# Performance work log

Measured on AMD Instinct MI355X. Metric: run time of the kernel, lower is better.

The kernel has to match this reference:

```python
import jax, jax.numpy as jnp
import numpy as np

D_MODEL = 1024
NUM_HEADS = 16
HEAD_DIM = D_MODEL // NUM_HEADS


def setup_inputs() -> dict:
    key = jax.random.key(0)
    ks = jax.random.split(key, 9)
    s = 1.0 / np.sqrt(D_MODEL)
    x = jax.random.normal(ks[0], (2, 2048, D_MODEL), dtype=jnp.float32)
    Wq = jax.random.uniform(ks[1], (D_MODEL, D_MODEL), jnp.float32, -s, s)
    bq = jax.random.uniform(ks[2], (D_MODEL,), jnp.float32, -s, s)
    Wk = jax.random.uniform(ks[3], (D_MODEL, D_MODEL), jnp.float32, -s, s)
    bk = jax.random.uniform(ks[4], (D_MODEL,), jnp.float32, -s, s)
    Wv = jax.random.uniform(ks[5], (D_MODEL, D_MODEL), jnp.float32, -s, s)
    bv = jax.random.uniform(ks[6], (D_MODEL,), jnp.float32, -s, s)
    Wo = jax.random.uniform(ks[7], (D_MODEL, D_MODEL), jnp.float32, -s, s)
    bo = jax.random.uniform(ks[8], (D_MODEL,), jnp.float32, -s, s)
    return {"x": x, "Wq": Wq, "bq": bq, "Wk": Wk, "bk": bk,
            "Wv": Wv, "bv": bv, "Wo": Wo, "bo": bo}


def reference(x, Wq, bq, Wk, bk, Wv, bv, Wo, bo):
    B, S, D = x.shape
    H, Hd = NUM_HEADS, HEAD_DIM
    # projections (torch Linear: x @ W.T + b; here W stored as [in, out])
    q = (x @ Wq + bq).reshape(B, S, H, Hd).transpose(0, 2, 1, 3)  # [B,H,S,Hd]
    k = (x @ Wk + bk).reshape(B, S, H, Hd).transpose(0, 2, 1, 3)
    v = (x @ Wv + bv).reshape(B, S, H, Hd).transpose(0, 2, 1, 3)
    scale = 1.0 / jnp.sqrt(jnp.asarray(Hd, dtype=x.dtype))
    scores = jnp.einsum('bhqd,bhkd->bhqk', q, k) * scale  # [B,H,S,S]
    attn = jax.nn.softmax(scores, axis=-1)
    out = jnp.einsum('bhqk,bhkd->bhqd', attn, v)  # [B,H,S,Hd]
    out = out.transpose(0, 2, 1, 3).reshape(B, S, D)
    return out @ Wo + bo
```

## Files before the change

kernel.cpp:

```cpp
#include <hip/hip_runtime.h>
#include <hip/hip_bf16.h>
#include <string.h>


#define DM 1024
#define S_LEN 2048
#define NH 16
#define HD 64

using u16 = unsigned short;
using u32 = unsigned int;

typedef short bf16x8 __attribute__((ext_vector_type(8)));
typedef float f32x4  __attribute__((ext_vector_type(4)));
typedef float f32x16 __attribute__((ext_vector_type(16)));
typedef unsigned int u32x2 __attribute__((ext_vector_type(2)));

__device__ __forceinline__ u16 f2bf(float f) {
    u32 i = __float_as_uint(f);
    u32 r = i + 0x7fffu + ((i >> 16) & 1u);
    return (u16)(r >> 16);
}
__device__ __forceinline__ u32 pk_bf16(float a, float b) {
    __hip_bfloat162 h = __float22bfloat162_rn(float2{a, b});
    u32 r; memcpy(&r, &h, 4);
    return r;
}

__global__ __launch_bounds__(256) void prep_x(const float* __restrict__ X, u16* __restrict__ out) {
    int i = (blockIdx.x * 256 + threadIdx.x) * 4;
    float4 v = *(const float4*)(X + i);
    *(uint2*)(out + i) = make_uint2(pk_bf16(v.x, v.y), pk_bf16(v.z, v.w));
}

__global__ __launch_bounds__(256) void prep_wt3(
    const float* __restrict__ W0, const float* __restrict__ W1, const float* __restrict__ W2,
    u16* __restrict__ T0, u16* __restrict__ T1, u16* __restrict__ T2)
{
    __shared__ u16 tile[64][72];
    const float* W = (blockIdx.z == 0) ? W0 : (blockIdx.z == 1) ? W1 : W2;
    u16* WT        = (blockIdx.z == 0) ? T0 : (blockIdx.z == 1) ? T1 : T2;
    const int t = threadIdx.x;
    const int n0 = blockIdx.x * 64, k0 = blockIdx.y * 64;
    #pragma unroll
    for (int it = 0; it < 4; it++) {
        int k = it * 16 + (t >> 4);
        int n = (t & 15) * 4;
        float4 v = *(const float4*)(W + (size_t)(k0 + k) * DM + n0 + n);
        tile[n + 0][k] = f2bf(v.x);
        tile[n + 1][k] = f2bf(v.y);
        tile[n + 2][k] = f2bf(v.z);
        tile[n + 3][k] = f2bf(v.w);
    }
    __syncthreads();
    int n = t >> 2, kg = (t & 3) * 16;
    uint4 a = *(const uint4*)&tile[n][kg];
    uint4 b = *(const uint4*)&tile[n][kg + 8];
    *(uint4*)(WT + (size_t)(n0 + n) * DM + k0 + kg)     = a;
    *(uint4*)(WT + (size_t)(n0 + n) * DM + k0 + kg + 8) = b;
}

__global__ __launch_bounds__(256) void prep_wt1(const float* __restrict__ W, u16* __restrict__ WT) {
    __shared__ u16 tile[64][72];
    const int t = threadIdx.x;
    const int n0 = blockIdx.x * 64, k0 = blockIdx.y * 64;
    #pragma unroll
    for (int it = 0; it < 4; it++) {
        int k = it * 16 + (t >> 4);
        int n = (t & 15) * 4;
        float4 v = *(const float4*)(W + (size_t)(k0 + k) * DM + n0 + n);
        tile[n + 0][k] = f2bf(v.x);
        tile[n + 1][k] = f2bf(v.y);
        tile[n + 2][k] = f2bf(v.z);
        tile[n + 3][k] = f2bf(v.w);
    }
    __syncthreads();
    int n = t >> 2, kg = (t & 3) * 16;
    uint4 a = *(const uint4*)&tile[n][kg];
    uint4 b = *(const uint4*)&tile[n][kg + 8];
    *(uint4*)(WT + (size_t)(n0 + n) * DM + k0 + kg)     = a;
    *(uint4*)(WT + (size_t)(n0 + n) * DM + k0 + kg + 8) = b;
}

__global__ __launch_bounds__(256) void gemm_qkv(
    const u16* __restrict__ WQT, const u16* __restrict__ WKT, const u16* __restrict__ WVT,
    const u16* __restrict__ X,
    const float* __restrict__ bq, const float* __restrict__ bk, const float* __restrict__ bv,
    u16* __restrict__ outQ, u16* __restrict__ outK, u16* __restrict__ outVT)
{
    __shared__ u16 Xs[128][72];
    __shared__ u16 Ws[3][64][72];

    const int t = threadIdx.x;
    const int w = t >> 6, lane = t & 63, quad = lane >> 4, l16 = lane & 15;
    const int Mb0 = blockIdx.x * 64;
    const int Nb0 = blockIdx.y * 128;
    const int Mb = Mb0 + (w & 1) * 32;
    const int Nb = Nb0 + (w >> 1) * 64;
    const int mloc = (w & 1) * 32, nloc = (w >> 1) * 64;

    f32x4 acc[3][2][4];
    #pragma unroll
    for (int q = 0; q < 3; q++)
        #pragma unroll
        for (int i = 0; i < 2; i++)
            #pragma unroll
            for (int j = 0; j < 4; j++) acc[q][i][j] = (f32x4){0.f, 0.f, 0.f, 0.f};

    const int sr = t >> 3, sc8 = (t & 7) * 8;

    for (int k0 = 0; k0 < DM; k0 += 64) {
        __syncthreads();
        #pragma unroll
        for (int i = 0; i < 4; i++) {
            int r = i * 32 + sr;
            *(uint4*)&Xs[r][sc8] =
                *(const uint4*)(X + (size_t)(Nb0 + r) * DM + k0 + sc8);
        }
        #pragma unroll
        for (int i = 0; i < 2; i++) {
            int r = i * 32 + sr;
            *(uint4*)&Ws[0][r][sc8] = *(const uint4*)(WQT + (size_t)(Mb0 + r) * DM + k0 + sc8);
            *(uint4*)&Ws[1][r][sc8] = *(const uint4*)(WKT + (size_t)(Mb0 + r) * DM + k0 + sc8);
            *(uint4*)&Ws[2][r][sc8] = *(const uint4*)(WVT + (size_t)(Mb0 + r) * DM + k0 + sc8);
        }
        __syncthreads();

        #pragma unroll
        for (int ks = 0; ks < 2; ks++) {
            const int kk = ks * 32 + quad * 8;
            bf16x8 bf[4];
            #pragma unroll
            for (int nt = 0; nt < 4; nt++)
                bf[nt] = *(const bf16x8*)&Xs[nloc + nt * 16 + l16][kk];
            bf16x8 aq0 = *(const bf16x8*)&Ws[0][mloc + l16][kk];
            bf16x8 aq1 = *(const bf16x8*)&Ws[0][mloc + 16 + l16][kk];
            bf16x8 ak0 = *(const bf16x8*)&Ws[1][mloc + l16][kk];
            bf16x8 ak1 = *(const bf16x8*)&Ws[1][mloc + 16 + l16][kk];
            bf16x8 av0 = *(const bf16x8*)&Ws[2][mloc + l16][kk];
            bf16x8 av1 = *(const bf16x8*)&Ws[2][mloc + 16 + l16][kk];
            #pragma unroll
            for (int nt = 0; nt < 4; nt++) {
                acc[0][0][nt] = __builtin_amdgcn_mfma_f32_16x16x32_bf16(aq0, bf[nt], acc[0][0][nt], 0, 0, 0);
                acc[0][1][nt] = __builtin_amdgcn_mfma_f32_16x16x32_bf16(aq1, bf[nt], acc[0][1][nt], 0, 0, 0);
                acc[1][0][nt] = __builtin_amdgcn_mfma_f32_16x16x32_bf16(ak0, bf[nt], acc[1][0][nt], 0, 0, 0);
                acc[1][1][nt] = __builtin_amdgcn_mfma_f32_16x16x32_bf16(ak1, bf[nt], acc[1][1][nt], 0, 0, 0);
                acc[2][0][nt] = __builtin_amdgcn_mfma_f32_16x16x32_bf16(av0, bf[nt], acc[2][0][nt], 0, 0, 0);
                acc[2][1][nt] = __builtin_amdgcn_mfma_f32_16x16x32_bf16(av1, bf[nt], acc[2][1][nt], 0, 0, 0);
            }
        }
    }

    const float QS = 0.18033688f;
    #pragma unroll
    for (int mt = 0; mt < 2; mt++) {
        int nf0 = Mb + mt * 16 + quad * 4;
        int h = nf0 >> 6, hd = nf0 & 63;
        float4 bvq = *(const float4*)(bq + nf0);
        float4 bvk = *(const float4*)(bk + nf0);
        #pragma unroll
        for (int nt = 0; nt < 4; nt++) {
            int m = Nb + nt * 16 + l16;
            int b = m >> 11, s = m & 2047;
            size_t idx = (size_t)(b * NH + h) * 131072 + (size_t)s * 64 + hd;
            *(uint2*)(outQ + idx) = make_uint2(
                pk_bf16((acc[0][mt][nt][0] + bvq.x) * QS, (acc[0][mt][nt][1] + bvq.y) * QS),
                pk_bf16((acc[0][mt][nt][2] + bvq.z) * QS, (acc[0][mt][nt][3] + bvq.w) * QS));
            *(uint2*)(outK + idx) = make_uint2(
                pk_bf16(acc[1][mt][nt][0] + bvk.x, acc[1][mt][nt][1] + bvk.y),
                pk_bf16(acc[1][mt][nt][2] + bvk.z, acc[1][mt][nt][3] + bvk.w));
        }
    }
    #pragma unroll
    for (int mt = 0; mt < 2; mt++) {
        #pragma unroll
        for (int r = 0; r < 4; r++) {
            int nf = Mb + mt * 16 + quad * 4 + r;
            int h = nf >> 6, hd = nf & 63;
            float bb = bv[nf];
            #pragma unroll
            for (int nt = 0; nt < 4; nt++) {
                int m = Nb + nt * 16 + l16;
                int b = m >> 11, s = m & 2047;
                outVT[(size_t)(b * NH + h) * 131072 + (size_t)hd * S_LEN + s]
                    = f2bf(acc[2][mt][nt][r] + bb);
            }
        }
    }
}

__global__ __launch_bounds__(256) void gemm_out(
    const u16* __restrict__ A, const u16* __restrict__ B,
    const float* __restrict__ bias, float* __restrict__ of32)
{
    __shared__ u16 As[64][72];
    __shared__ u16 Bs[128][72];

    const int t = threadIdx.x;
    const int w = t >> 6, lane = t & 63, quad = lane >> 4, l16 = lane & 15;
    const int Mb0 = blockIdx.x * 64;
    const int Nb0 = blockIdx.y * 128;
    const int Mb = Mb0 + (w & 1) * 32;
    const int Nb = Nb0 + (w >> 1) * 64;
    const int mloc = (w & 1) * 32, nloc = (w >> 1) * 64;

    f32x4 acc[2][4];
    #pragma unroll
    for (int i = 0; i < 2; i++)
        #pragma unroll
        for (int j = 0; j < 4; j++) acc[i][j] = (f32x4){0.f, 0.f, 0.f, 0.f};

    const int sr = t >> 3, sc8 = (t & 7) * 8;

    for (int k0 = 0; k0 < DM; k0 += 64) {
        const int h = k0 >> 6;
        __syncthreads();
        #pragma unroll
        for (int i = 0; i < 2; i++) {
            int r = i * 32 + sr;
            *(uint4*)&As[r][sc8] = *(const uint4*)(A + (size_t)(Mb0 + r) * DM + k0 + sc8);
        }
        #pragma unroll
        for (int i = 0; i < 4; i++) {
            int r = i * 32 + sr;
            int m = Nb0 + r;
            int b = m >> 11, s = m & 2047;
            *(uint4*)&Bs[r][sc8] =
                *(const uint4*)(B + (size_t)(b * NH + h) * 131072 + (size_t)s * 64 + sc8);
        }
        __syncthreads();

        #pragma unroll
        for (int ks = 0; ks < 2; ks++) {
            const int kk = ks * 32 + quad * 8;
            bf16x8 a0 = *(const bf16x8*)&As[mloc + l16][kk];
            bf16x8 a1 = *(const bf16x8*)&As[mloc + 16 + l16][kk];
            #pragma unroll
            for (int nt = 0; nt < 4; nt++) {
                bf16x8 bf = *(const bf16x8*)&Bs[nloc + nt * 16 + l16][kk];
                acc[0][nt] = __builtin_amdgcn_mfma_f32_16x16x32_bf16(a0, bf, acc[0][nt], 0, 0, 0);
                acc[1][nt] = __builtin_amdgcn_mfma_f32_16x16x32_bf16(a1, bf, acc[1][nt], 0, 0, 0);
            }
        }
    }
    #pragma unroll
    for (int mt = 0; mt < 2; mt++) {
        int nf0 = Mb + mt * 16 + quad * 4;
        float4 bvv = *(const float4*)(bias + nf0);
        #pragma unroll
        for (int nt = 0; nt < 4; nt++) {
            int m = Nb + nt * 16 + l16;
            float4 o;
            o.x = acc[mt][nt][0] + bvv.x; o.y = acc[mt][nt][1] + bvv.y;
            o.z = acc[mt][nt][2] + bvv.z; o.w = acc[mt][nt][3] + bvv.w;
            *(float4*)(of32 + (size_t)m * DM + nf0) = o;
        }
    }
}

__global__ __launch_bounds__(256) void attn_mfma(
    const u16* __restrict__ Q, const u16* __restrict__ K, const u16* __restrict__ VT,
    u16* __restrict__ O)
{
    __shared__ u16 Ks[2][64][72];
    __shared__ u16 Vs[2][64][72];

    const int t = threadIdx.x;
    const int w = t >> 6, lane = t & 63;
    const int l32 = lane & 31, h = lane >> 5;
    const int bh = blockIdx.y;
    const int q0 = blockIdx.x * 128;
    const size_t base = (size_t)bh * 131072;

    const int qrow = q0 + w * 32 + l32;
    bf16x8 qf[4];
    #pragma unroll
    for (int ks = 0; ks < 4; ks++)
        qf[ks] = *(const bf16x8*)(Q + base + (size_t)qrow * 64 + ks * 16 + h * 8);

    const short onebf = (short)0x3F80;
    const bf16x8 ones = {onebf, onebf, onebf, onebf, onebf, onebf, onebf, onebf};

    f32x16 o[2], lacc;
    #pragma unroll
    for (int ht = 0; ht < 2; ht++)
        #pragma unroll
        for (int i = 0; i < 16; i++) o[ht][i] = 0.f;
    #pragma unroll
    for (int i = 0; i < 16; i++) lacc[i] = 0.f;

    const int sr = t >> 3;
    const int sc8 = (t & 7) * 8;
    const u16* Kg = K + base;
    const u16* Vg = VT + base;

    #pragma unroll
    for (int i = 0; i < 2; i++) {
        int r = i * 32 + sr;
        *(uint4*)&Ks[0][r][sc8] = *(const uint4*)(Kg + (size_t)r * 64 + sc8);
        *(uint4*)&Vs[0][r][sc8] = *(const uint4*)(Vg + (size_t)r * S_LEN + sc8);
    }
    __syncthreads();

    for (int kt = 0; kt < 32; kt++) {
        const int cur = kt & 1;
        uint4 kreg[2], vreg[2];
        if (kt < 31) {
            #pragma unroll
            for (int i = 0; i < 2; i++) {
                int r = i * 32 + sr;
                kreg[i] = *(const uint4*)(Kg + (size_t)((kt + 1) * 64 + r) * 64 + sc8);
                vreg[i] = *(const uint4*)(Vg + (size_t)r * S_LEN + (kt + 1) * 64 + sc8);
            }
        }

        #pragma unroll
        for (int kh = 0; kh < 2; kh++) {
            f32x16 s;
            #pragma unroll
            for (int i = 0; i < 16; i++) s[i] = 0.f;
            #pragma unroll
            for (int ks = 0; ks < 4; ks++) {
                bf16x8 kf = *(const bf16x8*)&Ks[cur][kh * 32 + l32][ks * 16 + h * 8];
                s = __builtin_amdgcn_mfma_f32_32x32x16_bf16(kf, qf[ks], s, 0, 0, 0);
            }
            float p[16];
            #pragma unroll
            for (int i = 0; i < 16; i++) p[i] = __builtin_amdgcn_exp2f(s[i]);
            u32 A0 = pk_bf16(p[0],  p[1]),  B0 = pk_bf16(p[2],  p[3]);
            u32 A1 = pk_bf16(p[4],  p[5]),  B1 = pk_bf16(p[6],  p[7]);
            u32 A2 = pk_bf16(p[8],  p[9]),  B2 = pk_bf16(p[10], p[11]);
            u32 A3 = pk_bf16(p[12], p[13]), B3 = pk_bf16(p[14], p[15]);
            u32x2 sA0 = __builtin_amdgcn_permlane32_swap(A0, A1, false, false);
            u32x2 sB0 = __builtin_amdgcn_permlane32_swap(B0, B1, false, false);
            u32x2 sA1 = __builtin_amdgcn_permlane32_swap(A2, A3, false, false);
            u32x2 sB1 = __builtin_amdgcn_permlane32_swap(B2, B3, false, false);
            union { bf16x8 v; u32 wd[4]; } fr0, fr1;
            fr0.wd[0] = sA0.x; fr0.wd[1] = sB0.x; fr0.wd[2] = sA0.y; fr0.wd[3] = sB0.y;
            fr1.wd[0] = sA1.x; fr1.wd[1] = sB1.x; fr1.wd[2] = sA1.y; fr1.wd[3] = sB1.y;

            lacc = __builtin_amdgcn_mfma_f32_32x32x16_bf16(fr0.v, ones, lacc, 0, 0, 0);
            lacc = __builtin_amdgcn_mfma_f32_32x32x16_bf16(fr1.v, ones, lacc, 0, 0, 0);

            #pragma unroll
            for (int ht = 0; ht < 2; ht++) {
                bf16x8 vf0 = *(const bf16x8*)&Vs[cur][ht * 32 + l32][kh * 32 + h * 8];
                o[ht] = __builtin_amdgcn_mfma_f32_32x32x16_bf16(fr0.v, vf0, o[ht], 0, 0, 0);
                bf16x8 vf1 = *(const bf16x8*)&Vs[cur][ht * 32 + l32][kh * 32 + 16 + h * 8];
                o[ht] = __builtin_amdgcn_mfma_f32_32x32x16_bf16(fr1.v, vf1, o[ht], 0, 0, 0);
            }
        }

        if (kt < 31) {
            #pragma unroll
            for (int i = 0; i < 2; i++) {
                int r = i * 32 + sr;
                *(uint4*)&Ks[cur ^ 1][r][sc8] = kreg[i];
                *(uint4*)&Vs[cur ^ 1][r][sc8] = vreg[i];
            }
        }
        __syncthreads();
    }

    float inv[16];
    #pragma unroll
    for (int r = 0; r < 16; r++) inv[r] = 1.0f / lacc[r];
    #pragma unroll
    for (int ht = 0; ht < 2; ht++)
        #pragma unroll
        for (int r = 0; r < 16; r++) {
            int q = q0 + w * 32 + (r & 3) + 8 * (r >> 2) + 4 * h;
            O[base + (size_t)q * 64 + ht * 32 + l32] = f2bf(o[ht][r] * inv[r]);
        }
}

extern "C" void kernel_launch(void* const* d_in, const int* in_sizes, int n_in,
                              void* d_out, int out_size, void* d_ws, size_t ws_size,
                              hipStream_t stream) {
    const float* x  = (const float*)d_in[0];
    const float* Wq = (const float*)d_in[1];
    const float* bq = (const float*)d_in[2];
    const float* Wk = (const float*)d_in[3];
    const float* bk = (const float*)d_in[4];
    const float* Wv = (const float*)d_in[5];
    const float* bv = (const float*)d_in[6];
    const float* Wo = (const float*)d_in[7];
    const float* bo = (const float*)d_in[8];
    float* out = (float*)d_out;

    u16* xbf = (u16*)d_out;
    u16* wqt = xbf + 4194304;
    u16* wkt = wqt + 1048576;
    u16* wvt = wkt + 1048576;

    u16* qws  = (u16*)d_ws;
    u16* kws  = qws + 4194304;
    u16* vtws = kws + 4194304;
    u16* wot  = kws;

    prep_x<<<4096, 256, 0, stream>>>(x, xbf);
    prep_wt3<<<dim3(16, 16, 3), 256, 0, stream>>>(Wq, Wk, Wv, wqt, wkt, wvt);

    gemm_qkv<<<dim3(16, 32), 256, 0, stream>>>(wqt, wkt, wvt, xbf, bq, bk, bv,
                                               qws, kws, vtws);

    attn_mfma<<<dim3(16, 32), 256, 0, stream>>>(qws, kws, vtws, qws);

    prep_wt1<<<dim3(16, 16), 256, 0, stream>>>(Wo, wot);
    gemm_out<<<dim3(16, 32), 256, 0, stream>>>(wot, qws, bo, out);
}
```

Baseline: 200.2 us.

## Load K and V fragments directly from global memory, dropping LDS staging

The attention kernel no longer stages K and V tiles through double-buffered shared memory with block-wide barriers. Each lane now loads its MFMA operand fragments straight from global memory (through L1/L2) every key tile. This removes the LDS writes, LDS reads and __syncthreads, and frees LDS for occupancy. In exchange, each of the four waves in a block refetches the same K/V data, which raises global and cache traffic and exposes load latency because there is no explicit prefetch.

```diff
diff --git a/kernel.cpp b/kernel.cpp
--- a/kernel.cpp
+++ b/kernel.cpp
@@ -262,9 +262,6 @@
     const u16* __restrict__ Q, const u16* __restrict__ K, const u16* __restrict__ VT,
     u16* __restrict__ O)
 {
-    __shared__ u16 Ks[2][64][72];
-    __shared__ u16 Vs[2][64][72];
-
     const int t = threadIdx.x;
     const int w = t >> 6, lane = t & 63;
     const int l32 = lane & 31, h = lane >> 5;
@@ -289,29 +286,23 @@
     #pragma unroll
     for (int i = 0; i < 16; i++) lacc[i] = 0.f;
 
-    const int sr = t >> 3;
-    const int sc8 = (t & 7) * 8;
-    const u16* Kg = K + base;
-    const u16* Vg = VT + base;
-
-    #pragma unroll
-    for (int i = 0; i < 2; i++) {
-        int r = i * 32 + sr;
-        *(uint4*)&Ks[0][r][sc8] = *(const uint4*)(Kg + (size_t)r * 64 + sc8);
-        *(uint4*)&Vs[0][r][sc8] = *(const uint4*)(Vg + (size_t)r * S_LEN + sc8);
-    }
-    __syncthreads();
+    const u16* Kp0 = K  + base + (size_t)l32 * 64 + h * 8;
+    const u16* Kp1 = Kp0 + 32 * 64;
+    const u16* Vp0 = VT + base + (size_t)l32 * S_LEN + h * 8;
+    const u16* Vp1 = Vp0 + (size_t)32 * S_LEN;
 
     for (int kt = 0; kt < 32; kt++) {
-        const int cur = kt & 1;
-        uint4 kreg[2], vreg[2];
-        if (kt < 31) {
-            #pragma unroll
-            for (int i = 0; i < 2; i++) {
-                int r = i * 32 + sr;
-                kreg[i] = *(const uint4*)(Kg + (size_t)((kt + 1) * 64 + r) * 64 + sc8);
-                vreg[i] = *(const uint4*)(Vg + (size_t)r * S_LEN + (kt + 1) * 64 + sc8);
-            }
+        bf16x8 kf0[4], kf1[4];
+        #pragma unroll
+        for (int ks = 0; ks < 4; ks++) {
+            kf0[ks] = *(const bf16x8*)(Kp0 + ks * 16);
+            kf1[ks] = *(const bf16x8*)(Kp1 + ks * 16);
+        }
+        bf16x8 vf0[4], vf1[4];
+        #pragma unroll
+        for (int c = 0; c < 4; c++) {
+            vf0[c] = *(const bf16x8*)(Vp0 + c * 16);
+            vf1[c] = *(const bf16x8*)(Vp1 + c * 16);
         }
 
         #pragma unroll
@@ -321,7 +312,7 @@
             for (int i = 0; i < 16; i++) s[i] = 0.f;
             #pragma unroll
             for (int ks = 0; ks < 4; ks++) {
-                bf16x8 kf = *(const bf16x8*)&Ks[cur][kh * 32 + l32][ks * 16 + h * 8];
+                bf16x8 kf = kh ? kf1[ks] : kf0[ks];
                 s = __builtin_amdgcn_mfma_f32_32x32x16_bf16(kf, qf[ks], s, 0, 0, 0);
             }
             float p[16];
@@ -342,24 +333,14 @@
             lacc = __builtin_amdgcn_mfma_f32_32x32x16_bf16(fr0.v, ones, lacc, 0, 0, 0);
             lacc = __builtin_amdgcn_mfma_f32_32x32x16_bf16(fr1.v, ones, lacc, 0, 0, 0);
 
-            #pragma unroll
-            for (int ht = 0; ht < 2; ht++) {
-                bf16x8 vf0 = *(const bf16x8*)&Vs[cur][ht * 32 + l32][kh * 32 + h * 8];
-                o[ht] = __builtin_amdgcn_mfma_f32_32x32x16_bf16(fr0.v, vf0, o[ht], 0, 0, 0);
-                bf16x8 vf1 = *(const bf16x8*)&Vs[cur][ht * 32 + l32][kh * 32 + 16 + h * 8];
-                o[ht] = __builtin_amdgcn_mfma_f32_32x32x16_bf16(fr1.v, vf1, o[ht], 0, 0, 0);
-            }
-        }
-
-        if (kt < 31) {
-            #pragma unroll
-            for (int i = 0; i < 2; i++) {
-                int r = i * 32 + sr;
-                *(uint4*)&Ks[cur ^ 1][r][sc8] = kreg[i];
-                *(uint4*)&Vs[cur ^ 1][r][sc8] = vreg[i];
-            }
-        }
-        __syncthreads();
+            o[0] = __builtin_amdgcn_mfma_f32_32x32x16_bf16(fr0.v, vf0[kh * 2 + 0], o[0], 0, 0, 0);
+            o[0] = __builtin_amdgcn_mfma_f32_32x32x16_bf16(fr1.v, vf0[kh * 2 + 1], o[0], 0, 0, 0);
+            o[1] = __builtin_amdgcn_mfma_f32_32x32x16_bf16(fr0.v, vf1[kh * 2 + 0], o[1], 0, 0, 0);
+            o[1] = __builtin_amdgcn_mfma_f32_32x32x16_bf16(fr1.v, vf1[kh * 2 + 1], o[1], 0, 0, 0);
+        }
+
+        Kp0 += 64 * 64; Kp1 += 64 * 64;
+        Vp0 += 64;      Vp1 += 64;
     }
 
     float inv[16];
```

New measurement: 267.8 us. +33.8%, slower.

## Split fused QKV GEMM across grid z with larger 128x128 tiles

Applied to the files above, without the earlier changes.

Replaces the fused QKV GEMM, in which each block computed 64 output features for Q, K and V together, with a kernel that picks one projection per blockIdx.z and computes a 128x128 tile per block. The grid grows from 512 to 768 blocks, accumulator registers per wave drop from 24 to 16 f32x4, and a launch-bounds occupancy hint of 3 is added. The intent is to improve occupancy and GPU fill. The cost is that the X tile is now loaded three times, once per projection, instead of being shared across Q, K and V.

```diff
diff --git a/kernel.cpp b/kernel.cpp
--- a/kernel.cpp
+++ b/kernel.cpp
@@ -82,30 +82,29 @@
     *(uint4*)(WT + (size_t)(n0 + n) * DM + k0 + kg + 8) = b;
 }
 
-__global__ __launch_bounds__(256) void gemm_qkv(
+__global__ __launch_bounds__(256, 3) void gemm_qkv_z(
     const u16* __restrict__ WQT, const u16* __restrict__ WKT, const u16* __restrict__ WVT,
     const u16* __restrict__ X,
     const float* __restrict__ bq, const float* __restrict__ bk, const float* __restrict__ bv,
     u16* __restrict__ outQ, u16* __restrict__ outK, u16* __restrict__ outVT)
 {
+    __shared__ u16 Ws[128][72];
     __shared__ u16 Xs[128][72];
-    __shared__ u16 Ws[3][64][72];
+
+    const int z = blockIdx.z;
+    const u16* WT = (z == 0) ? WQT : (z == 1) ? WKT : WVT;
 
     const int t = threadIdx.x;
     const int w = t >> 6, lane = t & 63, quad = lane >> 4, l16 = lane & 15;
-    const int Mb0 = blockIdx.x * 64;
+    const int Mb0 = blockIdx.x * 128;
     const int Nb0 = blockIdx.y * 128;
-    const int Mb = Mb0 + (w & 1) * 32;
-    const int Nb = Nb0 + (w >> 1) * 64;
-    const int mloc = (w & 1) * 32, nloc = (w >> 1) * 64;
-
-    f32x4 acc[3][2][4];
-    #pragma unroll
-    for (int q = 0; q < 3; q++)
-        #pragma unroll
-        for (int i = 0; i < 2; i++)
-            #pragma unroll
-            for (int j = 0; j < 4; j++) acc[q][i][j] = (f32x4){0.f, 0.f, 0.f, 0.f};
+    const int mloc = (w & 1) * 64, nloc = (w >> 1) * 64;
+
+    f32x4 acc[4][4];
+    #pragma unroll
+    for (int i = 0; i < 4; i++)
+        #pragma unroll
+        for (int j = 0; j < 4; j++) acc[i][j] = (f32x4){0.f, 0.f, 0.f, 0.f};
 
     const int sr = t >> 3, sc8 = (t & 7) * 8;
 
@@ -114,76 +113,64 @@
         #pragma unroll
         for (int i = 0; i < 4; i++) {
             int r = i * 32 + sr;
-            *(uint4*)&Xs[r][sc8] =
-                *(const uint4*)(X + (size_t)(Nb0 + r) * DM + k0 + sc8);
-        }
-        #pragma unroll
-        for (int i = 0; i < 2; i++) {
-            int r = i * 32 + sr;
-            *(uint4*)&Ws[0][r][sc8] = *(const uint4*)(WQT + (size_t)(Mb0 + r) * DM + k0 + sc8);
-            *(uint4*)&Ws[1][r][sc8] = *(const uint4*)(WKT + (size_t)(Mb0 + r) * DM + k0 + sc8);
-            *(uint4*)&Ws[2][r][sc8] = *(const uint4*)(WVT + (size_t)(Mb0 + r) * DM + k0 + sc8);
+            *(uint4*)&Ws[r][sc8] = *(const uint4*)(WT + (size_t)(Mb0 + r) * DM + k0 + sc8);
+            *(uint4*)&Xs[r][sc8] = *(const uint4*)(X  + (size_t)(Nb0 + r) * DM + k0 + sc8);
         }
         __syncthreads();
 
         #pragma unroll
         for (int ks = 0; ks < 2; ks++) {
             const int kk = ks * 32 + quad * 8;
-            bf16x8 bf[4];
+            bf16x8 af[4], bf[4];
+            #pragma unroll
+            for (int mt = 0; mt < 4; mt++)
+                af[mt] = *(const bf16x8*)&Ws[mloc + mt * 16 + l16][kk];
             #pragma unroll
             for (int nt = 0; nt < 4; nt++)
                 bf[nt] = *(const bf16x8*)&Xs[nloc + nt * 16 + l16][kk];
-            bf16x8 aq0 = *(const bf16x8*)&Ws[0][mloc + l16][kk];
-            bf16x8 aq1 = *(const bf16x8*)&Ws[0][mloc + 16 + l16][kk];
-            bf16x8 ak0 = *(const bf16x8*)&Ws[1][mloc + l16][kk];
-            bf16x8 ak1 = *(const bf16x8*)&Ws[1][mloc + 16 + l16][kk];
-            bf16x8 av0 = *(const bf16x8*)&Ws[2][mloc + l16][kk];
-            bf16x8 av1 = *(const bf16x8*)&Ws[2][mloc + 16 + l16][kk];
+            #pragma unroll
+            for (int mt = 0; mt < 4; mt++)
+                #pragma unroll
+                for (int nt = 0; nt < 4; nt++)
+                    acc[mt][nt] = __builtin_amdgcn_mfma_f32_16x16x32_bf16(af[mt], bf[nt], acc[mt][nt], 0, 0, 0);
+        }
+    }
+
+    const float QS = 0.18033688f;
+    if (z <= 1) {
+        u16* outP = (z == 0) ? outQ : outK;
+        const float* bias = (z == 0) ? bq : bk;
+        const float scale = (z == 0) ? QS : 1.0f;
+        #pragma unroll
+        for (int mt = 0; mt < 4; mt++) {
+            int nf0 = Mb0 + mloc + mt * 16 + quad * 4;
+            int hh = nf0 >> 6, hd = nf0 & 63;
+            float4 bb = *(const float4*)(bias + nf0);
             #pragma unroll
             for (int nt = 0; nt < 4; nt++) {
-                acc[0][0][nt] = __builtin_amdgcn_mfma_f32_16x16x32_bf16(aq0, bf[nt], acc[0][0][nt], 0, 0, 0);
-                acc[0][1][nt] = __builtin_amdgcn_mfma_f32_16x16x32_bf16(aq1, bf[nt], acc[0][1][nt], 0, 0, 0);
-                acc[1][0][nt] = __builtin_amdgcn_mfma_f32_16x16x32_bf16(ak0, bf[nt], acc[1][0][nt], 0, 0, 0);
-                acc[1][1][nt] = __builtin_amdgcn_mfma_f32_16x16x32_bf16(ak1, bf[nt], acc[1][1][nt], 0, 0, 0);
-                acc[2][0][nt] = __builtin_amdgcn_mfma_f32_16x16x32_bf16(av0, bf[nt], acc[2][0][nt], 0, 0, 0);
-                acc[2][1][nt] = __builtin_amdgcn_mfma_f32_16x16x32_bf16(av1, bf[nt], acc[2][1][nt], 0, 0, 0);
-            }
-        }
-    }
-
-    const float QS = 0.18033688f;
-    #pragma unroll
-    for (int mt = 0; mt < 2; mt++) {
-        int nf0 = Mb + mt * 16 + quad * 4;
-        int h = nf0 >> 6, hd = nf0 & 63;
-        float4 bvq = *(const float4*)(bq + nf0);
-        float4 bvk = *(const float4*)(bk + nf0);
-        #pragma unroll
-        for (int nt = 0; nt < 4; nt++) {
-            int m = Nb + nt * 16 + l16;
-            int b = m >> 11, s = m & 2047;
-            size_t idx = (size_t)(b * NH + h) * 131072 + (size_t)s * 64 + hd;
-            *(uint2*)(outQ + idx) = make_uint2(
-                pk_bf16((acc[0][mt][nt][0] + bvq.x) * QS, (acc[0][mt][nt][1] + bvq.y) * QS),
-                pk_bf16((acc[0][mt][nt][2] + bvq.z) * QS, (acc[0][mt][nt][3] + bvq.w) * QS));
-            *(uint2*)(outK + idx) = make_uint2(
-                pk_bf16(acc[1][mt][nt][0] + bvk.x, acc[1][mt][nt][1] + bvk.y),
-                pk_bf16(acc[1][mt][nt][2] + bvk.z, acc[1][mt][nt][3] + bvk.w));
-        }
-    }
-    #pragma unroll
-    for (int mt = 0; mt < 2; mt++) {
-        #pragma unroll
-        for (int r = 0; r < 4; r++) {
-            int nf = Mb + mt * 16 + quad * 4 + r;
-            int h = nf >> 6, hd = nf & 63;
-            float bb = bv[nf];
-            #pragma unroll
-            for (int nt = 0; nt < 4; nt++) {
-                int m = Nb + nt * 16 + l16;
+                int m = Nb0 + nloc + nt * 16 + l16;
                 int b = m >> 11, s = m & 2047;
-                outVT[(size_t)(b * NH + h) * 131072 + (size_t)hd * S_LEN + s]
-                    = f2bf(acc[2][mt][nt][r] + bb);
+                size_t idx = (size_t)(b * NH + hh) * 131072 + (size_t)s * 64 + hd;
+                *(uint2*)(outP + idx) = make_uint2(
+                    pk_bf16((acc[mt][nt][0] + bb.x) * scale, (acc[mt][nt][1] + bb.y) * scale),
+                    pk_bf16((acc[mt][nt][2] + bb.z) * scale, (acc[mt][nt][3] + bb.w) * scale));
+            }
+        }
+    } else {
+        #pragma unroll
+        for (int mt = 0; mt < 4; mt++) {
+            #pragma unroll
+            for (int r = 0; r < 4; r++) {
+                int nf = Mb0 + mloc + mt * 16 + quad * 4 + r;
+                int hh = nf >> 6, hd = nf & 63;
+                float bb = bv[nf];
+                #pragma unroll
+                for (int nt = 0; nt < 4; nt++) {
+                    int m = Nb0 + nloc + nt * 16 + l16;
+                    int b = m >> 11, s = m & 2047;
+                    outVT[(size_t)(b * NH + hh) * 131072 + (size_t)hd * S_LEN + s]
+                        = f2bf(acc[mt][nt][r] + bb);
+                }
             }
         }
     }
@@ -401,8 +388,8 @@
     prep_x<<<4096, 256, 0, stream>>>(x, xbf);
     prep_wt3<<<dim3(16, 16, 3), 256, 0, stream>>>(Wq, Wk, Wv, wqt, wkt, wvt);
 
-    gemm_qkv<<<dim3(16, 32), 256, 0, stream>>>(wqt, wkt, wvt, xbf, bq, bk, bv,
-                                               qws, kws, vtws);
+    gemm_qkv_z<<<dim3(8, 32, 3), 256, 0, stream>>>(wqt, wkt, wvt, xbf, bq, bk, bv,
+                                                   qws, kws, vtws);
 
     attn_mfma<<<dim3(16, 32), 256, 0, stream>>>(qws, kws, vtws, qws);
 
```

Result: no change. 198.9 us (-0.6%).
